# Performance work log

Hardware: AMD Instinct MI355X
Metric: run time of the kernel (lower is better)

Reference implementation:

```python
import jax, jax.numpy as jnp
import numpy as np

EMBED_DIM = 256
NUM_HEADS = 8
HEAD_DIM = EMBED_DIM // NUM_HEADS
WINDOW = 31
B, S = 4, 2048


def _make_params(key):
    ks = jax.random.split(key, 8)
    sc = 0.05
    Wq = jax.random.normal(ks[0], (NUM_HEADS, EMBED_DIM, HEAD_DIM), jnp.float32) * sc
    bq = jax.random.normal(ks[1], (NUM_HEADS, HEAD_DIM), jnp.float32) * sc
    Wk = jax.random.normal(ks[2], (NUM_HEADS, EMBED_DIM, HEAD_DIM), jnp.float32) * sc
    bk = jax.random.normal(ks[3], (NUM_HEADS, HEAD_DIM), jnp.float32) * sc
    Wv = jax.random.normal(ks[4], (NUM_HEADS, EMBED_DIM, HEAD_DIM), jnp.float32) * sc
    bv = jax.random.normal(ks[5], (NUM_HEADS, HEAD_DIM), jnp.float32) * sc
    Wo = jax.random.normal(ks[6], (NUM_HEADS * HEAD_DIM, EMBED_DIM), jnp.float32) * sc
    bo = jax.random.normal(ks[7], (EMBED_DIM,), jnp.float32) * sc
    return Wq, bq, Wk, bk, Wv, bv, Wo, bo


def setup_inputs() -> dict:
    key = jax.random.key(0)
    k1, k2, k3, k4 = jax.random.split(key, 4)
    eeg = jax.random.normal(k1, (B, S, EMBED_DIM), jnp.float32)
    pps = jax.random.normal(k2, (B, S, EMBED_DIM), jnp.float32)
    e2p = _make_params(k3)
    p2e = _make_params(k4)
    names = ["Wq", "bq", "Wk", "bk", "Wv", "bv", "Wo", "bo"]
    inp = {"eeg": eeg, "pps": pps}
    for n, p in zip(names, e2p):
        inp["e2p_" + n] = p
    for n, p in zip(names, p2e):
        inp["p2e_" + n] = p
    return inp


def _cross_window_attn(q_seq, kv_seq, Wq, bq, Wk, bk, Wv, bv, Wo, bo, window):
    # q_seq, kv_seq: [B, S, D]. Each query position i attends to window of
    # the zero-padded kv sequence centered at i (pad positions get bias-only k/v,
    # matching torch Linear applied to zero vectors).
    b, s, d_in = q_seq.shape
    h, _, hd = Wq.shape
    pad = (window - 1) // 2
    kv_pad = jnp.pad(kv_seq, ((0, 0), (pad, pad), (0, 0)))
    Q = jnp.einsum('bsd,hde->bhse', q_seq, Wq) + bq[None, :, None, :]
    K = jnp.einsum('bsd,hde->bhse', kv_pad, Wk) + bk[None, :, None, :]
    V = jnp.einsum('bsd,hde->bhse', kv_pad, Wv) + bv[None, :, None, :]
    idx = jnp.arange(s)[:, None] + jnp.arange(window)[None, :]  # [S, W]
    Kw = K[:, :, idx, :]  # [B, H, S, W, hd]
    Vw = V[:, :, idx, :]
    scores = jnp.einsum('bhse,bhswe->bhsw', Q, Kw) / np.sqrt(hd).astype(np.float32)
    attn = jax.nn.softmax(scores, axis=-1)
    out = jnp.einsum('bhsw,bhswe->bhse', attn, Vw)  # [B, H, S, hd]
    out = out.transpose(0, 2, 1, 3).reshape(b, s, h * hd)
    return out @ Wo + bo


def reference(eeg, pps,
              e2p_Wq, e2p_bq, e2p_Wk, e2p_bk, e2p_Wv, e2p_bv, e2p_Wo, e2p_bo,
              p2e_Wq, p2e_bq, p2e_Wk, p2e_bk, p2e_Wv, p2e_bv, p2e_Wo, p2e_bo):
    fused_eeg = _cross_window_attn(eeg, pps, e2p_Wq, e2p_bq, e2p_Wk, e2p_bk,
                                   e2p_Wv, e2p_bv, e2p_Wo, e2p_bo, WINDOW)
    fused_pps = _cross_window_attn(pps, eeg, p2e_Wq, p2e_bq, p2e_Wk, p2e_bk,
                                   p2e_Wv, p2e_bv, p2e_Wo, p2e_bo, WINDOW)
    return fused_eeg, fused_pps
```

## Files before the change

kernel.cpp:

```cpp
#include <hip/hip_runtime.h>

static __device__ __forceinline__ float bf2f(unsigned short u) {
    return __uint_as_float(((unsigned int)u) << 16);
}
static __device__ __forceinline__ unsigned short f2bf(float f) {
    unsigned int x = __float_as_uint(f);
    unsigned int lsb = (x >> 16) & 1u;
    x += 0x7fffu + lsb;
    return (unsigned short)(x >> 16);
}

typedef __attribute__((ext_vector_type(8))) short short8;
typedef __attribute__((ext_vector_type(4))) float floatx4;

static __device__ __forceinline__ short8 ldg8(const unsigned short* p) {
    short8 v; __builtin_memcpy(&v, p, 16); return v;
}


__global__ __launch_bounds__(256) void repack_kernel(
    const float* e2p_Wq, const float* e2p_bq,
    const float* e2p_Wk, const float* e2p_bk,
    const float* e2p_Wv, const float* e2p_bv,
    const float* e2p_Wo, const float* e2p_bo,
    const float* p2e_Wq, const float* p2e_bq,
    const float* p2e_Wk, const float* p2e_bk,
    const float* p2e_Wv, const float* p2e_bv,
    const float* p2e_Wo, const float* p2e_bo,
    const float* eeg, const float* pps,
    unsigned short* Wpack, unsigned short* Wopack, float* bias_pack, float* bias2,
    unsigned short* Abf)
{
    __shared__ unsigned short tr[2048];
    const int bid = blockIdx.x, tid = threadIdx.x;

    if (bid < 2048) {
        const int g = bid >> 1, kc_half = (bid & 1) * 4;
        const int inp = g >> 9;
        const int m = (g & 511) * 16 + (tid >> 4);
        const int k8 = kc_half * 4 + (tid & 15);
        const float* src = inp ? pps : eeg;
        float v[8];
        __builtin_memcpy(v, src + (long)m * 256 + k8 * 8, 32);
        unsigned short o[8];
        #pragma unroll
        for (int j = 0; j < 8; ++j) o[j] = f2bf(v[j]);
        const int k8l = tid & 15;
        __builtin_memcpy(&tr[(k8l >> 2) * 512 + ((k8l & 3) * 16 + (tid >> 4)) * 8], o, 16);
        __syncthreads();
        unsigned short t[8];
        __builtin_memcpy(t, &tr[tid * 8], 16);
        __builtin_memcpy(Abf + inp * 2097152 + ((g & 511) * 8 + kc_half) * 512 + tid * 8, t, 16);
        return;
    }
    if (bid < 2240) {
        int idx = (bid - 2048) * 256 + tid;
        int inp = idx / 24576, r = idx % 24576;
        int n = (r & 15) | ((r >> 9) << 4);
        int k8 = (r >> 4) & 31;
        int kc = k8 >> 2, q4 = k8 & 3, kb = k8 * 8;
        int proj = n / 256, h = (n % 256) / 32, e = n % 32;
        const float* W;
        if (inp == 0) W = (proj == 0) ? e2p_Wq : (proj == 1) ? p2e_Wk : p2e_Wv;
        else          W = (proj == 0) ? p2e_Wq : (proj == 1) ? e2p_Wk : e2p_Wv;
        unsigned short o[8];
        #pragma unroll
        for (int j = 0; j < 8; ++j) o[j] = f2bf(W[h * 8192 + (kb + j) * 32 + e]);
        __builtin_memcpy(Wpack + inp * 196608 + ((n >> 4) * 8 + kc) * 512 + (q4 * 16 + (n & 15)) * 8, o, 16);
        return;
    }
    if (bid < 2304) {
        int i2 = (bid - 2240) * 256 + tid;
        int dir = i2 / 8192, r = i2 % 8192;
        int n = (r & 15) | ((r >> 9) << 4);
        int k8 = (r >> 4) & 31;
        int kc = k8 >> 2, q4 = k8 & 3, kb = k8 * 8;
        const float* Wo = dir ? p2e_Wo : e2p_Wo;
        unsigned short o[8];
        #pragma unroll
        for (int j = 0; j < 8; ++j) o[j] = f2bf(Wo[(kb + j) * 256 + n]);
        __builtin_memcpy(Wopack + dir * 65536 + ((n >> 4) * 8 + kc) * 512 + (q4 * 16 + (n & 15)) * 8, o, 16);
        return;
    }
    {
        int idx = (bid - 2304) * 256 + tid;
        if (idx < 1536) {
            int inp = idx / 768, n = idx % 768;
            int proj = n / 256, he = n % 256;
            const float* bsrc;
            if (inp == 0) bsrc = (proj == 0) ? e2p_bq : (proj == 1) ? p2e_bk : p2e_bv;
            else          bsrc = (proj == 0) ? p2e_bq : (proj == 1) ? e2p_bk : e2p_bv;
            bias_pack[idx] = bsrc[he];
        } else {
            int j = idx - 1536;
            int dir = j / 256, n = j % 256;
            bias2[j] = (dir == 0 ? e2p_bo : p2e_bo)[n];
        }
    }
}

__global__ __launch_bounds__(256) void mfma_gemm_kernel(
    const unsigned short* __restrict__ A0, const unsigned short* __restrict__ A1,
    const unsigned short* __restrict__ B0f, const unsigned short* __restrict__ B1f,
    const float* __restrict__ bias0, const float* __restrict__ bias1,
    unsigned short* __restrict__ C0, unsigned short* __restrict__ C1,
    int N)
{
    __shared__ __align__(16) unsigned short Cs[128][136];

    const int z = blockIdx.z;
    const unsigned short* A = z ? A1 : A0;
    const unsigned short* Bf = z ? B1f : B0f;
    const float* bias = z ? bias1 : bias0;
    unsigned short* C = z ? C1 : C0;

    const int tid = threadIdx.x;
    const long m0 = (long)blockIdx.x * 128;
    const int n0 = blockIdx.y * 128;

    const int lane = tid & 63;
    const int wv = tid >> 6;
    const int wm = (wv >> 1) * 64, wn = (wv & 1) * 64;
    const int fr = lane & 15, q4 = lane >> 4;

    const unsigned short* Aw = A + ((blockIdx.x * 8 + (wm >> 4)) * 8) * 512 + lane * 8;
    const unsigned short* Bw = Bf + ((blockIdx.y * 8 + (wn >> 4)) * 8) * 512 + lane * 8;

    floatx4 acc[4][4] = {};
    short8 af[2][4], bf_[2][4];

    #pragma unroll
    for (int i = 0; i < 4; ++i) af[0][i] = ldg8(Aw + i * 4096);
    #pragma unroll
    for (int j = 0; j < 4; ++j) bf_[0][j] = ldg8(Bw + j * 4096);

    #pragma unroll
    for (int kc = 0; kc < 8; ++kc) {
        const int cur = kc & 1, nxt = cur ^ 1;
        if (kc < 7) {
            #pragma unroll
            for (int i = 0; i < 4; ++i) af[nxt][i] = ldg8(Aw + (i * 8 + kc + 1) * 512);
            #pragma unroll
            for (int j = 0; j < 4; ++j) bf_[nxt][j] = ldg8(Bw + (j * 8 + kc + 1) * 512);
        }
        #pragma unroll
        for (int i = 0; i < 4; ++i)
            #pragma unroll
            for (int j = 0; j < 4; ++j)
                acc[i][j] = __builtin_amdgcn_mfma_f32_16x16x32_bf16(af[cur][i], bf_[cur][j], acc[i][j], 0, 0, 0);
    }

    float bj[4];
    #pragma unroll
    for (int j = 0; j < 4; ++j) bj[j] = bias[n0 + wn + j * 16 + fr];

    const int cr0 = wm + (q4 << 2);
    #pragma unroll
    for (int i = 0; i < 4; ++i)
        #pragma unroll
        for (int j = 0; j < 4; ++j)
            #pragma unroll
            for (int r = 0; r < 4; ++r)
                Cs[cr0 + i * 16 + r][wn + j * 16 + fr] = f2bf(acc[i][j][r] + bj[j]);
    __syncthreads();

    const int rr = tid >> 4, cc = (tid & 15) * 8;
    #pragma unroll
    for (int p = 0; p < 8; ++p) {
        int r = p * 16 + rr;
        unsigned short tmp[8];
        __builtin_memcpy(tmp, &Cs[r][cc], 16);
        __builtin_memcpy(C + (m0 + r) * N + n0 + cc, tmp, 16);
    }
}

#define KROWS 48
#define VROWS 64
#define KVSTR 264
__global__ __launch_bounds__(512) void attn_out_kernel(
    const unsigned short* __restrict__ Y, const float* __restrict__ bias_pack,
    const unsigned short* __restrict__ Wopack, const float* __restrict__ bias2,
    float* __restrict__ out)
{
    __shared__ __align__(16) unsigned short smem[(KROWS + VROWS) * KVSTR];
    unsigned short* Ks = smem;
    unsigned short* Vs = smem + KROWS * KVSTR;
    unsigned short (*Ps)[16][72] = (unsigned short(*)[16][72])smem;
    unsigned short (*As)[KVSTR] = (unsigned short(*)[KVSTR])smem;
    float (*Os)[264] = (float(*)[264])smem;

    const int s0 = blockIdx.x * 16;
    const int b = blockIdx.y, dir = blockIdx.z;
    const int kvinp = 1 - dir;
    const int tid = threadIdx.x;

    const float* bkv = bias_pack + kvinp * 768;
    const long kvbase = ((long)kvinp * 8192 + b * 2048) * 768;

    {
        const int r = tid >> 3, seg = (tid & 7) * 32;
        int p = s0 - 15 + r;
        unsigned short vr[32];
        if (p >= 0 && p < 2048) {
            __builtin_memcpy(vr, Y + kvbase + (long)p * 768 + 512 + seg, 64);
        } else {
            #pragma unroll
            for (int j = 0; j < 32; ++j) vr[j] = f2bf(bkv[512 + seg + j]);
        }
        __builtin_memcpy(&Vs[r * KVSTR + seg], vr, 64);
        if (tid < 384) {
            unsigned short kr[32];
            if (p >= 0 && p < 2048) {
                __builtin_memcpy(kr, Y + kvbase + (long)p * 768 + 256 + seg, 64);
            } else {
                #pragma unroll
                for (int j = 0; j < 32; ++j) kr[j] = f2bf(bkv[256 + seg + j]);
            }
            __builtin_memcpy(&Ks[r * KVSTR + seg], kr, 64);
        }
    }

    const int lane = tid & 63;
    const int wv = tid >> 6;
    const int fr = lane & 15, q4 = lane >> 4;
    short8 aq = ldg8(Y + ((long)dir * 8192 + b * 2048 + s0 + fr) * 768 + wv * 32 + q4 * 8);

    __syncthreads();

    floatx4 sacc[3] = {};
    #pragma unroll
    for (int kvt = 0; kvt < 3; ++kvt) {
        short8 bk_ = *(const short8*)&Ks[(kvt * 16 + fr) * KVSTR + wv * 32 + q4 * 8];
        sacc[kvt] = __builtin_amdgcn_mfma_f32_16x16x32_bf16(aq, bk_, sacc[kvt], 0, 0, 0);
    }

    float sv[3][4];
    float mx[4] = {-3.0e38f, -3.0e38f, -3.0e38f, -3.0e38f};
    #pragma unroll
    for (int kvt = 0; kvt < 3; ++kvt)
        #pragma unroll
        for (int reg = 0; reg < 4; ++reg) {
            int i = q4 * 4 + reg;
            int jc = kvt * 16 + fr;
            int d = jc - i;
            float x = (d >= 0 && d <= 30) ? sacc[kvt][reg] * 0.17677669529663687f : -3.0e38f;
            sv[kvt][reg] = x;
            mx[reg] = fmaxf(mx[reg], x);
        }
    #pragma unroll
    for (int off = 1; off < 16; off <<= 1)
        #pragma unroll
        for (int reg = 0; reg < 4; ++reg)
            mx[reg] = fmaxf(mx[reg], __shfl_xor(mx[reg], off));
    float ps[4] = {};
    #pragma unroll
    for (int kvt = 0; kvt < 3; ++kvt)
        #pragma unroll
        for (int reg = 0; reg < 4; ++reg) {
            float e = __expf(sv[kvt][reg] - mx[reg]);
            sv[kvt][reg] = e;
            ps[reg] += e;
        }
    #pragma unroll
    for (int off = 1; off < 16; off <<= 1)
        #pragma unroll
        for (int reg = 0; reg < 4; ++reg)
            ps[reg] += __shfl_xor(ps[reg], off);

    __syncthreads();

    #pragma unroll
    for (int reg = 0; reg < 4; ++reg) {
        int i = q4 * 4 + reg;
        #pragma unroll
        for (int kvt = 0; kvt < 3; ++kvt)
            Ps[wv][i][kvt * 16 + fr] = f2bf(sv[kvt][reg]);
        Ps[wv][i][48 + fr] = 0;
    }

    floatx4 oacc[2] = {};
    #pragma unroll
    for (int ch = 0; ch < 2; ++ch) {
        short8 ap = *(const short8*)&Ps[wv][fr][ch * 32 + q4 * 8];
        #pragma unroll
        for (int et = 0; et < 2; ++et) {
            short8 bv;
            #pragma unroll
            for (int j = 0; j < 8; ++j)
                bv[j] = (short)Vs[(ch * 32 + q4 * 8 + j) * KVSTR + wv * 32 + et * 16 + fr];
            oacc[et] = __builtin_amdgcn_mfma_f32_16x16x32_bf16(ap, bv, oacc[et], 0, 0, 0);
        }
    }

    float rs[4];
    #pragma unroll
    for (int reg = 0; reg < 4; ++reg) rs[reg] = 1.0f / ps[reg];

    __syncthreads();

    #pragma unroll
    for (int et = 0; et < 2; ++et)
        #pragma unroll
        for (int reg = 0; reg < 4; ++reg)
            As[q4 * 4 + reg][wv * 32 + et * 16 + fr] = f2bf(oacc[et][reg] * rs[reg]);

    __syncthreads();

    const unsigned short* Wo = Wopack + dir * 65536 + lane * 8;
    const int nw = wv * 32;
    floatx4 oa[2] = {};
    #pragma unroll
    for (int kc = 0; kc < 8; ++kc) {
        short8 ap = *(const short8*)&As[fr][kc * 32 + q4 * 8];
        #pragma unroll
        for (int j = 0; j < 2; ++j) {
            short8 bw = ldg8(Wo + ((wv * 2 + j) * 8 + kc) * 512);
            oa[j] = __builtin_amdgcn_mfma_f32_16x16x32_bf16(ap, bw, oa[j], 0, 0, 0);
        }
    }

    float bj[2];
    #pragma unroll
    for (int j = 0; j < 2; ++j) bj[j] = bias2[dir * 256 + nw + j * 16 + fr];

    __syncthreads();

    #pragma unroll
    for (int j = 0; j < 2; ++j)
        #pragma unroll
        for (int reg = 0; reg < 4; ++reg)
            Os[q4 * 4 + reg][nw + j * 16 + fr] = oa[j][reg] + bj[j];

    __syncthreads();

    const int row = tid >> 5, col = (tid & 31) * 8;
    float t8[8];
    __builtin_memcpy(t8, &Os[row][col], 32);
    __builtin_memcpy(out + (long)dir * 2097152 + ((long)b * 2048 + s0 + row) * 256 + col, t8, 32);
}

extern "C" void kernel_launch(void* const* d_in, const int* in_sizes, int n_in,
                              void* d_out, int out_size, void* d_ws, size_t ws_size,
                              hipStream_t stream)
{
    float* out = (float*)d_out;

    char* ws = (char*)d_ws;
    unsigned short* Wpack   = (unsigned short*)(ws + 0);
    unsigned short* Wopack  = (unsigned short*)(ws + 786432);
    float*          biasP   = (float*)(ws + 1048576);
    float*          bias2   = (float*)(ws + 1054720);
    unsigned short* Y       = (unsigned short*)(ws + 1056768);
    unsigned short* Abf     = (unsigned short*)(ws + 26222592);

    repack_kernel<<<2312, 256, 0, stream>>>(
        (const float*)d_in[2],  (const float*)d_in[3],
        (const float*)d_in[4],  (const float*)d_in[5],
        (const float*)d_in[6],  (const float*)d_in[7],
        (const float*)d_in[8],  (const float*)d_in[9],
        (const float*)d_in[10], (const float*)d_in[11],
        (const float*)d_in[12], (const float*)d_in[13],
        (const float*)d_in[14], (const float*)d_in[15],
        (const float*)d_in[16], (const float*)d_in[17],
        (const float*)d_in[0],  (const float*)d_in[1],
        Wpack, Wopack, biasP, bias2, Abf);

    mfma_gemm_kernel<<<dim3(64, 6, 2), 256, 0, stream>>>(
        Abf, Abf + 2097152, Wpack, Wpack + 196608, biasP, biasP + 768,
        Y, Y + 8192 * 768, 768);

    attn_out_kernel<<<dim3(128, 4, 2), 512, 0, stream>>>(Y, biasP, Wopack, bias2, out);
}
```

Before: 140.1 us.

## Process 32 query rows per attention block to reuse K/V window and Wo loads

The attention+output-projection kernel now handles 32 query positions per block instead of 16, halving the grid. The loaded K/V window of 64 rows is shared by two 16-row query tiles, and each Wo fragment loaded from global memory feeds two MFMAs. The output staging through LDS is removed in favour of direct scattered float stores, and launch bounds now request 4 waves per SIMD. The costs are more registers and LDS per block, fewer blocks (512) to fill the GPU, and less coalesced output writes.

Measured after the change: 131.8 us. 1.06x faster.

```diff
diff --git a/kernel.cpp b/kernel.cpp
--- a/kernel.cpp
+++ b/kernel.cpp
@@ -174,22 +174,20 @@
     }
 }
 
-#define KROWS 48
-#define VROWS 64
 #define KVSTR 264
-__global__ __launch_bounds__(512) void attn_out_kernel(
+#define PSTR 72
+__global__ __launch_bounds__(512, 4) void attn_out_kernel(
     const unsigned short* __restrict__ Y, const float* __restrict__ bias_pack,
     const unsigned short* __restrict__ Wopack, const float* __restrict__ bias2,
     float* __restrict__ out)
 {
-    __shared__ __align__(16) unsigned short smem[(KROWS + VROWS) * KVSTR];
+    __shared__ __align__(16) unsigned short smem[18432 + 16896];
     unsigned short* Ks = smem;
-    unsigned short* Vs = smem + KROWS * KVSTR;
-    unsigned short (*Ps)[16][72] = (unsigned short(*)[16][72])smem;
-    unsigned short (*As)[KVSTR] = (unsigned short(*)[KVSTR])smem;
-    float (*Os)[264] = (float(*)[264])smem;
-
-    const int s0 = blockIdx.x * 16;
+    unsigned short* Vs = smem + 18432;
+    unsigned short (*Ps)[32][PSTR] = (unsigned short(*)[32][PSTR])smem;
+    unsigned short (*As)[KVSTR] = (unsigned short(*)[KVSTR])(smem + 18432);
+
+    const int s0 = blockIdx.x * 32;
     const int b = blockIdx.y, dir = blockIdx.z;
     const int kvinp = 1 - dir;
     const int tid = threadIdx.x;
@@ -199,123 +197,132 @@
 
     {
         const int r = tid >> 3, seg = (tid & 7) * 32;
-        int p = s0 - 15 + r;
-        unsigned short vr[32];
+        const int p = s0 - 15 + r;
+        unsigned short tmp[32];
         if (p >= 0 && p < 2048) {
-            __builtin_memcpy(vr, Y + kvbase + (long)p * 768 + 512 + seg, 64);
+            __builtin_memcpy(tmp, Y + kvbase + (long)p * 768 + 256 + seg, 64);
         } else {
             #pragma unroll
-            for (int j = 0; j < 32; ++j) vr[j] = f2bf(bkv[512 + seg + j]);
-        }
-        __builtin_memcpy(&Vs[r * KVSTR + seg], vr, 64);
-        if (tid < 384) {
-            unsigned short kr[32];
-            if (p >= 0 && p < 2048) {
-                __builtin_memcpy(kr, Y + kvbase + (long)p * 768 + 256 + seg, 64);
-            } else {
-                #pragma unroll
-                for (int j = 0; j < 32; ++j) kr[j] = f2bf(bkv[256 + seg + j]);
-            }
-            __builtin_memcpy(&Ks[r * KVSTR + seg], kr, 64);
-        }
+            for (int j = 0; j < 32; ++j) tmp[j] = f2bf(bkv[256 + seg + j]);
+        }
+        __builtin_memcpy(&Ks[r * KVSTR + seg], tmp, 64);
+        if (p >= 0 && p < 2048) {
+            __builtin_memcpy(tmp, Y + kvbase + (long)p * 768 + 512 + seg, 64);
+        } else {
+            #pragma unroll
+            for (int j = 0; j < 32; ++j) tmp[j] = f2bf(bkv[512 + seg + j]);
+        }
+        __builtin_memcpy(&Vs[r * KVSTR + seg], tmp, 64);
     }
 
     const int lane = tid & 63;
     const int wv = tid >> 6;
     const int fr = lane & 15, q4 = lane >> 4;
-    short8 aq = ldg8(Y + ((long)dir * 8192 + b * 2048 + s0 + fr) * 768 + wv * 32 + q4 * 8);
+    short8 aq[2];
+    #pragma unroll
+    for (int it = 0; it < 2; ++it)
+        aq[it] = ldg8(Y + ((long)dir * 8192 + b * 2048 + s0 + it * 16 + fr) * 768 + wv * 32 + q4 * 8);
 
     __syncthreads();
 
-    floatx4 sacc[3] = {};
-    #pragma unroll
-    for (int kvt = 0; kvt < 3; ++kvt) {
+    floatx4 sacc[2][3] = {};
+    #pragma unroll
+    for (int kvt = 0; kvt < 4; ++kvt) {
         short8 bk_ = *(const short8*)&Ks[(kvt * 16 + fr) * KVSTR + wv * 32 + q4 * 8];
-        sacc[kvt] = __builtin_amdgcn_mfma_f32_16x16x32_bf16(aq, bk_, sacc[kvt], 0, 0, 0);
-    }
-
-    float sv[3][4];
-    float mx[4] = {-3.0e38f, -3.0e38f, -3.0e38f, -3.0e38f};
-    #pragma unroll
-    for (int kvt = 0; kvt < 3; ++kvt)
+        if (kvt < 3) sacc[0][kvt]     = __builtin_amdgcn_mfma_f32_16x16x32_bf16(aq[0], bk_, sacc[0][kvt], 0, 0, 0);
+        if (kvt > 0) sacc[1][kvt - 1] = __builtin_amdgcn_mfma_f32_16x16x32_bf16(aq[1], bk_, sacc[1][kvt - 1], 0, 0, 0);
+    }
+
+    float sv[2][3][4];
+    float rs[2][4];
+    #pragma unroll
+    for (int it = 0; it < 2; ++it) {
+        float mx[4] = {-3.0e38f, -3.0e38f, -3.0e38f, -3.0e38f};
+        #pragma unroll
+        for (int kt = 0; kt < 3; ++kt)
+            #pragma unroll
+            for (int reg = 0; reg < 4; ++reg) {
+                int i = it * 16 + q4 * 4 + reg;
+                int jc = (it + kt) * 16 + fr;
+                int d = jc - i;
+                float x = (d >= 0 && d <= 30) ? sacc[it][kt][reg] * 0.17677669529663687f : -3.0e38f;
+                sv[it][kt][reg] = x;
+                mx[reg] = fmaxf(mx[reg], x);
+            }
+        #pragma unroll
+        for (int off = 1; off < 16; off <<= 1)
+            #pragma unroll
+            for (int reg = 0; reg < 4; ++reg)
+                mx[reg] = fmaxf(mx[reg], __shfl_xor(mx[reg], off));
+        float ps[4] = {};
+        #pragma unroll
+        for (int kt = 0; kt < 3; ++kt)
+            #pragma unroll
+            for (int reg = 0; reg < 4; ++reg) {
+                float e = __expf(sv[it][kt][reg] - mx[reg]);
+                sv[it][kt][reg] = e;
+                ps[reg] += e;
+            }
+        #pragma unroll
+        for (int off = 1; off < 16; off <<= 1)
+            #pragma unroll
+            for (int reg = 0; reg < 4; ++reg)
+                ps[reg] += __shfl_xor(ps[reg], off);
+        #pragma unroll
+        for (int reg = 0; reg < 4; ++reg) rs[it][reg] = 1.0f / ps[reg];
+    }
+
+    __syncthreads();
+
+    #pragma unroll
+    for (int it = 0; it < 2; ++it)
         #pragma unroll
         for (int reg = 0; reg < 4; ++reg) {
-            int i = q4 * 4 + reg;
-            int jc = kvt * 16 + fr;
-            int d = jc - i;
-            float x = (d >= 0 && d <= 30) ? sacc[kvt][reg] * 0.17677669529663687f : -3.0e38f;
-            sv[kvt][reg] = x;
-            mx[reg] = fmaxf(mx[reg], x);
-        }
-    #pragma unroll
-    for (int off = 1; off < 16; off <<= 1)
-        #pragma unroll
-        for (int reg = 0; reg < 4; ++reg)
-            mx[reg] = fmaxf(mx[reg], __shfl_xor(mx[reg], off));
-    float ps[4] = {};
-    #pragma unroll
-    for (int kvt = 0; kvt < 3; ++kvt)
-        #pragma unroll
-        for (int reg = 0; reg < 4; ++reg) {
-            float e = __expf(sv[kvt][reg] - mx[reg]);
-            sv[kvt][reg] = e;
-            ps[reg] += e;
-        }
-    #pragma unroll
-    for (int off = 1; off < 16; off <<= 1)
-        #pragma unroll
-        for (int reg = 0; reg < 4; ++reg)
-            ps[reg] += __shfl_xor(ps[reg], off);
-
-    __syncthreads();
-
-    #pragma unroll
-    for (int reg = 0; reg < 4; ++reg) {
-        int i = q4 * 4 + reg;
-        #pragma unroll
-        for (int kvt = 0; kvt < 3; ++kvt)
-            Ps[wv][i][kvt * 16 + fr] = f2bf(sv[kvt][reg]);
-        Ps[wv][i][48 + fr] = 0;
-    }
-
-    floatx4 oacc[2] = {};
+            int i = it * 16 + q4 * 4 + reg;
+            #pragma unroll
+            for (int kt = 0; kt < 3; ++kt)
+                Ps[wv][i][(it + kt) * 16 + fr] = f2bf(sv[it][kt][reg]);
+            Ps[wv][i][(it == 0 ? 48 : 0) + fr] = 0;
+        }
+
+    floatx4 oacc[2][2] = {};
     #pragma unroll
     for (int ch = 0; ch < 2; ++ch) {
-        short8 ap = *(const short8*)&Ps[wv][fr][ch * 32 + q4 * 8];
+        short8 ap0 = *(const short8*)&Ps[wv][fr][ch * 32 + q4 * 8];
+        short8 ap1 = *(const short8*)&Ps[wv][16 + fr][ch * 32 + q4 * 8];
         #pragma unroll
         for (int et = 0; et < 2; ++et) {
             short8 bv;
             #pragma unroll
             for (int j = 0; j < 8; ++j)
                 bv[j] = (short)Vs[(ch * 32 + q4 * 8 + j) * KVSTR + wv * 32 + et * 16 + fr];
-            oacc[et] = __builtin_amdgcn_mfma_f32_16x16x32_bf16(ap, bv, oacc[et], 0, 0, 0);
-        }
-    }
-
-    float rs[4];
-    #pragma unroll
-    for (int reg = 0; reg < 4; ++reg) rs[reg] = 1.0f / ps[reg];
-
-    __syncthreads();
-
-    #pragma unroll
-    for (int et = 0; et < 2; ++et)
-        #pragma unroll
-        for (int reg = 0; reg < 4; ++reg)
-            As[q4 * 4 + reg][wv * 32 + et * 16 + fr] = f2bf(oacc[et][reg] * rs[reg]);
+            oacc[0][et] = __builtin_amdgcn_mfma_f32_16x16x32_bf16(ap0, bv, oacc[0][et], 0, 0, 0);
+            oacc[1][et] = __builtin_amdgcn_mfma_f32_16x16x32_bf16(ap1, bv, oacc[1][et], 0, 0, 0);
+        }
+    }
+
+    #pragma unroll
+    for (int it = 0; it < 2; ++it)
+        #pragma unroll
+        for (int et = 0; et < 2; ++et)
+            #pragma unroll
+            for (int reg = 0; reg < 4; ++reg)
+                As[it * 16 + q4 * 4 + reg][wv * 32 + et * 16 + fr] = f2bf(oacc[it][et][reg] * rs[it][reg]);
 
     __syncthreads();
 
     const unsigned short* Wo = Wopack + dir * 65536 + lane * 8;
     const int nw = wv * 32;
-    floatx4 oa[2] = {};
+    floatx4 oa[2][2] = {};
     #pragma unroll
     for (int kc = 0; kc < 8; ++kc) {
-        short8 ap = *(const short8*)&As[fr][kc * 32 + q4 * 8];
+        short8 ap0 = *(const short8*)&As[fr][kc * 32 + q4 * 8];
+        short8 ap1 = *(const short8*)&As[16 + fr][kc * 32 + q4 * 8];
         #pragma unroll
         for (int j = 0; j < 2; ++j) {
             short8 bw = ldg8(Wo + ((wv * 2 + j) * 8 + kc) * 512);
-            oa[j] = __builtin_amdgcn_mfma_f32_16x16x32_bf16(ap, bw, oa[j], 0, 0, 0);
+            oa[0][j] = __builtin_amdgcn_mfma_f32_16x16x32_bf16(ap0, bw, oa[0][j], 0, 0, 0);
+            oa[1][j] = __builtin_amdgcn_mfma_f32_16x16x32_bf16(ap1, bw, oa[1][j], 0, 0, 0);
         }
     }
 
@@ -323,20 +330,14 @@
     #pragma unroll
     for (int j = 0; j < 2; ++j) bj[j] = bias2[dir * 256 + nw + j * 16 + fr];
 
-    __syncthreads();
-
-    #pragma unroll
-    for (int j = 0; j < 2; ++j)
-        #pragma unroll
-        for (int reg = 0; reg < 4; ++reg)
-            Os[q4 * 4 + reg][nw + j * 16 + fr] = oa[j][reg] + bj[j];
-
-    __syncthreads();
-
-    const int row = tid >> 5, col = (tid & 31) * 8;
-    float t8[8];
-    __builtin_memcpy(t8, &Os[row][col], 32);
-    __builtin_memcpy(out + (long)dir * 2097152 + ((long)b * 2048 + s0 + row) * 256 + col, t8, 32);
+    float* obase = out + (long)dir * 2097152 + ((long)b * 2048 + s0) * 256;
+    #pragma unroll
+    for (int it = 0; it < 2; ++it)
+        #pragma unroll
+        for (int j = 0; j < 2; ++j)
+            #pragma unroll
+            for (int reg = 0; reg < 4; ++reg)
+                obase[(it * 16 + q4 * 4 + reg) * 256 + nw + j * 16 + fr] = oa[it][j][reg] + bj[j];
 }
 
 extern "C" void kernel_launch(void* const* d_in, const int* in_sizes, int n_in,
@@ -369,5 +370,5 @@
         Abf, Abf + 2097152, Wpack, Wpack + 196608, biasP, biasP + 768,
         Y, Y + 8192 * 768, 768);
 
-    attn_out_kernel<<<dim3(128, 4, 2), 512, 0, stream>>>(Y, biasP, Wopack, bias2, out);
-}
+    attn_out_kernel<<<dim3(64, 4, 2), 512, 0, stream>>>(Y, biasP, Wopack, bias2, out);
+}
```
